# Kernel optimization log

Hardware: AMD Instinct MI355X
Metric: run time of the kernel (lower is better)

The kernel has to match this reference:

```python
import jax, jax.numpy as jnp
import numpy as np
import math

N_EMB = 256
N_HEAD = 8
B_SEGS = 128
T_SEG = 256  # equal-length segments; N = B_SEGS * T_SEG


def setup_inputs() -> dict:
    key = jax.random.key(0)
    ks = jax.random.split(key, 10)
    N = B_SEGS * T_SEG
    x = jax.random.normal(ks[0], (N, N_EMB), dtype=jnp.float32)
    batch = jnp.repeat(jnp.arange(B_SEGS, dtype=jnp.int64), T_SEG)
    s = 1.0 / math.sqrt(N_EMB)
    def lin(k):
        kw, kb = jax.random.split(k)
        W = jax.random.uniform(kw, (N_EMB, N_EMB), jnp.float32, -s, s)
        b = jax.random.uniform(kb, (N_EMB,), jnp.float32, -s, s)
        return W, b
    Wq, bq = lin(ks[1])
    Wk, bk = lin(ks[2])
    Wv, bv = lin(ks[3])
    Wp, bp = lin(ks[4])
    return {"x": x, "batch": batch, "Wq": Wq, "bq": bq, "Wk": Wk, "bk": bk,
            "Wv": Wv, "bv": bv, "Wp": Wp, "bp": bp}


def reference(x, batch, Wq, bq, Wk, bk, Wv, bv, Wp, bp):
    # Dropout layers are identity in eval / p=0.
    N, C = x.shape
    H = N_HEAD
    hd = C // H
    B = int(batch[-1]) + 1        # equal-length segments
    T = N // B
    xr = x.reshape(B, T, C)
    # per-segment QKV projections: [B,H,T,hd]
    def heads(W, b):
        return (xr @ W.T + b).reshape(B, T, H, hd).transpose(0, 2, 1, 3)
    q = heads(Wq, bq)
    k = heads(Wk, bk)
    v = heads(Wv, bv)
    scores = jnp.einsum('bhtd,bhsd->bhts', q, k) * (1.0 / math.sqrt(hd))
    attn = jax.nn.softmax(scores, axis=-1)          # [B,H,T,T]
    y = jnp.einsum('bhts,bhsd->bhtd', attn, v)      # [B,H,T,hd]
    y = y.transpose(0, 2, 1, 3).reshape(B, T, C)
    y = y @ Wp.T + bp
    attn_mean = attn.mean(axis=1)                   # head-mean per segment [B,T,T]
    return y.reshape(N, C), attn_mean
```

## Files before the change

### kernel.cpp

```cpp
#include <hip/hip_runtime.h>
#include <hip/hip_bf16.h>
#include <stdint.h>

typedef unsigned short u16;
typedef __bf16 bf16_t;
typedef bf16_t bf16x8 __attribute__((ext_vector_type(8)));
typedef float f32x4 __attribute__((ext_vector_type(4)));

#define NTOK 32768
#define CEMB 256
#define NHEAD 8
#define HD 32
#define BSEG 128
#define TSEG 256

static __device__ __forceinline__ bf16x8 ld16(const u16* p) {
  uint4 v = *reinterpret_cast<const uint4*>(p);
  return __builtin_bit_cast(bf16x8, v);
}
static __device__ __forceinline__ u16 f2b(float f) {
  return __builtin_bit_cast(u16, (bf16_t)f);
}

typedef __attribute__((address_space(1))) const void GASV;
typedef __attribute__((address_space(3))) void LASV;
static __device__ __forceinline__ void stage16(const u16* g, u16* l) {
  __builtin_amdgcn_global_load_lds((GASV*)g, (LASV*)l, 16, 0, 0);
}

__global__ void k_convert(const float* __restrict__ x,
                          const float* __restrict__ wq, const float* __restrict__ wk,
                          const float* __restrict__ wv, const float* __restrict__ wp,
                          u16* __restrict__ xb, u16* __restrict__ wb) {
  const int XSLOTS = (NTOK * CEMB) / 8;
  const int WSLOTS = (4 * CEMB * CEMB) / 8;
  int slot = blockIdx.x * blockDim.x + threadIdx.x;
  if (slot >= XSLOTS + WSLOTS) return;
  const float* src;
  u16* dst;
  if (slot < XSLOTS) {
    src = x + slot * 8;
    dst = xb + slot * 8;
  } else {
    int e = (slot - XSLOTS) * 8;
    int wsel = e >> 16, off = e & 65535;
    const float* s0 = (wsel == 0) ? wq : ((wsel == 1) ? wk : ((wsel == 2) ? wv : wp));
    src = s0 + off;
    dst = wb + e;
  }
  float4 a = reinterpret_cast<const float4*>(src)[0];
  float4 b = reinterpret_cast<const float4*>(src)[1];
  u16 o[8] = {f2b(a.x), f2b(a.y), f2b(a.z), f2b(a.w),
              f2b(b.x), f2b(b.y), f2b(b.z), f2b(b.w)};
  *reinterpret_cast<uint4*>(dst) = *reinterpret_cast<const uint4*>(o);
}

#define GEMM_MAIN_LOOP(Asrc, Bsrc)                                              \
  f32x4 acc[4][4];                                                              \
  _Pragma("unroll") for (int mf = 0; mf < 4; ++mf)                              \
      _Pragma("unroll") for (int nf = 0; nf < 4; ++nf) {                        \
    f32x4 z = {0.f, 0.f, 0.f, 0.f};                                             \
    acc[mf][nf] = z;                                                            \
  }                                                                             \
  u16* As = lds;                                                                \
  u16* Bs = lds + 16384;                                                        \
  auto STAGE = [&](int buf, int kt) {                                           \
    _Pragma("unroll") for (int i = 0; i < 4; ++i) {                             \
      int cidx = i * 256 + tid;                                                 \
      int row = cidx >> 3;                                                      \
      int scb = ((cidx & 7) << 4) ^ ((row & 7) << 4);        \
      u16* dst_lds = As + buf * 8192 + (i * 256 + w * 64) * 8;                  \
      stage16(Asrc + (size_t)(m0 + row) * CEMB + kt * 64 + (scb >> 1), dst_lds);\
      u16* dst_ldsb = Bs + buf * 8192 + (i * 256 + w * 64) * 8;                 \
      stage16(Bsrc + (size_t)(n0 + row) * CEMB + kt * 64 + (scb >> 1), dst_ldsb);\
    }                                                                           \
  };                                                                            \
  STAGE(0, 0);                                                                  \
  __syncthreads();                                                              \
  for (int kt = 0; kt < 4; ++kt) {                                              \
    int buf = kt & 1;                                                           \
    if (kt < 3) STAGE(buf ^ 1, kt + 1);                                         \
    bf16x8 av[4][2], bw[4][2];                                                  \
    _Pragma("unroll") for (int mf = 0; mf < 4; ++mf)                            \
        _Pragma("unroll") for (int kk = 0; kk < 2; ++kk) {                      \
      int row = wr * 64 + mf * 16 + lr;                                         \
      int byte = row * 128 + ((kk * 64 + lg * 16) ^ ((row & 7) << 4));          \
      av[mf][kk] = *reinterpret_cast<const bf16x8*>(                            \
          (const char*)(As + buf * 8192) + byte);                               \
    }                                                                           \
    _Pragma("unroll") for (int nf = 0; nf < 4; ++nf)                            \
        _Pragma("unroll") for (int kk = 0; kk < 2; ++kk) {                      \
      int row = wc * 64 + nf * 16 + lr;                                         \
      int byte = row * 128 + ((kk * 64 + lg * 16) ^ ((row & 7) << 4));          \
      bw[nf][kk] = *reinterpret_cast<const bf16x8*>(                            \
          (const char*)(Bs + buf * 8192) + byte);                               \
    }                                                                           \
    _Pragma("unroll") for (int kk = 0; kk < 2; ++kk)                            \
        _Pragma("unroll") for (int nf = 0; nf < 4; ++nf)                        \
            _Pragma("unroll") for (int mf = 0; mf < 4; ++mf)                    \
      acc[mf][nf] = __builtin_amdgcn_mfma_f32_16x16x32_bf16(                    \
          av[mf][kk], bw[nf][kk], acc[mf][nf], 0, 0, 0);                        \
    __syncthreads();                                                            \
  }

__global__ __launch_bounds__(256, 2)
void k_qkv(const u16* __restrict__ xb, const u16* __restrict__ wb,
           const float* __restrict__ bq, const float* __restrict__ bk,
           const float* __restrict__ bv,
           u16* __restrict__ q_ws, u16* __restrict__ k_ws, u16* __restrict__ v_ws) {
  const int d = blockIdx.x;
  const int xcd = d & 7, i = d >> 3;
  const int m_idx = xcd * 32 + i / 6;
  const int rr = i % 6;
  const int mode = rr >> 1;
  const int n0 = (rr & 1) * 128;
  const int m0 = m_idx * 128;
  const int tid = threadIdx.x;
  const int w = tid >> 6, l = tid & 63;
  const int lr = l & 15, lg = l >> 4;
  const int wr = w >> 1, wc = w & 1;

  __shared__ u16 lds[32768];

  const u16* W = wb + mode * (CEMB * CEMB);
  const float* bias = (mode == 0) ? bq : ((mode == 1) ? bk : bv);

  GEMM_MAIN_LOOP(xb, W)

  float bb[4];
#pragma unroll
  for (int nf = 0; nf < 4; ++nf) bb[nf] = bias[n0 + wc * 64 + nf * 16 + lr];

  if (mode < 2) {
    u16* Et = lds;
#pragma unroll
    for (int mf = 0; mf < 4; ++mf)
#pragma unroll
      for (int nf = 0; nf < 4; ++nf)
#pragma unroll
        for (int r = 0; r < 4; ++r) {
          int row = wr * 64 + mf * 16 + lg * 4 + r;
          int col = wc * 64 + nf * 16 + lr;
          int byte = (row * 256 + col * 2) ^ ((row & 7) << 4);
          *(u16*)((char*)Et + byte) = f2b(acc[mf][nf][r] + bb[nf]);
        }
    __syncthreads();
    u16* out = (mode == 0) ? q_ws : k_ws;
    int row_l = tid >> 1, half = tid & 1;
    u16* dstp = out + (size_t)(m0 + row_l) * CEMB + n0 + half * 64;
#pragma unroll
    for (int j = 0; j < 8; ++j) {
      int byte = row_l * 256 + (((half * 64 + j * 8) * 2) ^ ((row_l & 7) << 4));
      *reinterpret_cast<uint4*>(dstp + j * 8) =
          *reinterpret_cast<const uint4*>((const char*)Et + byte);
    }
  } else {
    u16* Vt = lds;
#pragma unroll
    for (int mf = 0; mf < 4; ++mf)
#pragma unroll
      for (int nf = 0; nf < 4; ++nf)
#pragma unroll
        for (int r = 0; r < 4; ++r) {
          int row = wr * 64 + mf * 16 + lg * 4 + r;
          int col = wc * 64 + nf * 16 + lr;
          int byte = (col * 256 + row * 2) ^ ((col & 7) << 4);
          *(u16*)((char*)Vt + byte) = f2b(acc[mf][nf][r] + bb[nf]);
        }
    __syncthreads();
    int col_l = tid >> 1, half = tid & 1;
    int c = n0 + col_l, hh = c >> 5, dd = c & 31;
    int bs = m0 >> 8, t0 = m0 & 255;
    u16* dst = v_ws + ((size_t)(bs * NHEAD + hh) * HD + dd) * TSEG + t0 + half * 64;
#pragma unroll
    for (int j = 0; j < 8; ++j) {
      int byte = col_l * 256 + ((half * 128 + j * 16) ^ ((col_l & 7) << 4));
      *reinterpret_cast<uint4*>(dst + j * 8) =
          *reinterpret_cast<const uint4*>((const char*)Vt + byte);
    }
  }
}

__global__ __launch_bounds__(512, 2)
void k_attn(const u16* __restrict__ q_ws, const u16* __restrict__ k_ws,
            const u16* __restrict__ v_ws,
            u16* __restrict__ y_ws, float* __restrict__ mean_out) {
  const int dblk = blockIdx.x;
  const int xcd = dblk & 7, ii = dblk >> 3;
  const int b = xcd * 16 + (ii >> 1);
  const int th = ii & 1;
  const int tid = threadIdx.x;
  const int w = tid >> 6, l = tid & 63;
  const int lr = l & 15, lg = l >> 4;
  const int tbase = th * 128 + w * 16;

  __shared__ u16 ldsKV[32768];

  float macc[16][4];
#pragma unroll
  for (int st = 0; st < 16; ++st)
#pragma unroll
    for (int r = 0; r < 4; ++r) macc[st][r] = 0.f;

  const float sc = 0.17677669529663687f * 1.4426950408889634f;

  const u16* qseg = q_ws + (size_t)b * TSEG * CEMB;
  const u16* kseg = k_ws + (size_t)b * TSEG * CEMB;
  const u16* vseg = v_ws + (size_t)(b * NHEAD) * HD * TSEG;

  auto STAGE_KV = [&](int hn, int bn) {
    u16* Kb = ldsKV + bn * 8192;
    u16* Vb = ldsKV + 16384 + bn * 8192;
#pragma unroll
    for (int r = 0; r < 2; ++r) {
      int idx = r * 512 + tid;
      int c = idx >> 6, l2 = idx & 63;
      int lr2 = l2 & 15, lg2 = l2 >> 4;
      int srow = 32 * (c >> 1) + 4 * (c & 1) + 8 * (lr2 >> 2) + (lr2 & 3);
      stage16(kseg + srow * CEMB + hn * HD + lg2 * 8, Kb + idx * 8);
      int vrow = (c >> 3) * 16 + lr2;
      int vcol = (c & 7) * 32 + lg2 * 8;
      stage16(vseg + (size_t)(hn * HD + vrow) * TSEG + vcol, Vb + idx * 8);
    }
  };

  STAGE_KV(0, 0);
  bf16x8 qf = ld16(qseg + (tbase + lr) * CEMB + lg * 8);

  for (int h = 0; h < NHEAD; ++h) {
    const int bn = h & 1;
    __syncthreads();
    if (h < 7) STAGE_KV(h + 1, bn ^ 1);
    const u16* Kb = ldsKV + bn * 8192;
    const u16* Vb = ldsKV + 16384 + bn * 8192;

    float s[16][4];
#pragma unroll
    for (int st = 0; st < 16; ++st) {
      bf16x8 kf = *reinterpret_cast<const bf16x8*>(Kb + (st * 64 + l) * 8);
      f32x4 z = {0.f, 0.f, 0.f, 0.f};
      f32x4 dd = __builtin_amdgcn_mfma_f32_16x16x32_bf16(kf, qf, z, 0, 0, 0);
#pragma unroll
      for (int r = 0; r < 4; ++r) s[st][r] = dd[r] * sc;
    }

    qf = ld16(qseg + (tbase + lr) * CEMB + ((h + 1) & 7) * HD + lg * 8);

    float mx = s[0][0];
#pragma unroll
    for (int st = 0; st < 16; ++st)
#pragma unroll
      for (int r = 0; r < 4; ++r) mx = fmaxf(mx, s[st][r]);
    mx = fmaxf(mx, __shfl_xor(mx, 16, 64));
    mx = fmaxf(mx, __shfl_xor(mx, 32, 64));

    float sm = 0.f;
#pragma unroll
    for (int st = 0; st < 16; ++st)
#pragma unroll
      for (int r = 0; r < 4; ++r) {
        float p = exp2f(s[st][r] - mx);
        s[st][r] = p;
        sm += p;
      }
    sm += __shfl_xor(sm, 16, 64);
    sm += __shfl_xor(sm, 32, 64);
    float inv = __builtin_amdgcn_rcpf(sm);

    bf16x8 pb[8];
#pragma unroll
    for (int kk = 0; kk < 8; ++kk)
#pragma unroll
      for (int e = 0; e < 4; ++e) {
        float p0 = s[2 * kk][e] * inv;
        float p1 = s[2 * kk + 1][e] * inv;
        macc[2 * kk][e] += p0;
        macc[2 * kk + 1][e] += p1;
        pb[kk][e] = (bf16_t)p0;
        pb[kk][4 + e] = (bf16_t)p1;
      }

#pragma unroll
    for (int dt = 0; dt < 2; ++dt) {
      f32x4 y = {0.f, 0.f, 0.f, 0.f};
#pragma unroll
      for (int kk = 0; kk < 8; ++kk) {
        bf16x8 vf = *reinterpret_cast<const bf16x8*>(Vb + ((dt * 8 + kk) * 64 + l) * 8);
        y = __builtin_amdgcn_mfma_f32_16x16x32_bf16(vf, pb[kk], y, 0, 0, 0);
      }
      u16 o[4] = {f2b(y[0]), f2b(y[1]), f2b(y[2]), f2b(y[3])};
      *reinterpret_cast<uint2*>(
          y_ws + (size_t)(b * TSEG + tbase + lr) * CEMB + h * HD + dt * 16 + lg * 4) =
          *reinterpret_cast<const uint2*>(o);
    }
  }

  __syncthreads();

  float* smem = reinterpret_cast<float*>(ldsKV);
  float* smw = smem + w * (16 * 65) + lr * 65;
  const int trow = l >> 2;
  const int cql = (l & 3) * 4;
  const float* srcp = smem + w * (16 * 65) + trow * 65 + cql;
  float* gdst = mean_out + (size_t)(b * TSEG + tbase + trow) * TSEG + cql;

  for (int c = 0; c < 4; ++c) {
#pragma unroll
    for (int j = 0; j < 2; ++j)
#pragma unroll
      for (int jj = 0; jj < 2; ++jj) {
        int st = 4 * c + 2 * j + jj;
        int sl = 32 * j + 4 * jj + 8 * lg;
#pragma unroll
        for (int r = 0; r < 4; ++r) smw[sl + r] = macc[st][r] * 0.125f;
      }
#pragma unroll
    for (int j = 0; j < 4; ++j)
      *reinterpret_cast<f32x4*>(gdst + c * 64 + j * 16) =
          *reinterpret_cast<const f32x4*>(srcp + j * 16);
  }
}

__global__ __launch_bounds__(256, 2)
void k_proj(const u16* __restrict__ yb, const u16* __restrict__ wb,
            const float* __restrict__ bp, float* __restrict__ out) {
  const int d = blockIdx.x;
  const int xcd = d & 7, i = d >> 3;
  const int m0 = (xcd * 32 + (i >> 1)) * 128;
  const int n0 = (i & 1) * 128;
  const int tid = threadIdx.x;
  const int w = tid >> 6, l = tid & 63;
  const int lr = l & 15, lg = l >> 4;
  const int wr = w >> 1, wc = w & 1;
  const u16* W = wb + 3 * (CEMB * CEMB);

  __shared__ u16 lds[32768];

  GEMM_MAIN_LOOP(yb, W)

  float bb[4];
#pragma unroll
  for (int nf = 0; nf < 4; ++nf) bb[nf] = bp[n0 + wc * 64 + nf * 16 + lr];
#pragma unroll
  for (int mf = 0; mf < 4; ++mf)
#pragma unroll
    for (int nf = 0; nf < 4; ++nf)
#pragma unroll
      for (int r = 0; r < 4; ++r) {
        int m = m0 + wr * 64 + mf * 16 + lg * 4 + r;
        int c = n0 + wc * 64 + nf * 16 + lr;
        out[(size_t)m * CEMB + c] = acc[mf][nf][r] + bb[nf];
      }
}

extern "C" void kernel_launch(void* const* d_in, const int* in_sizes, int n_in,
                              void* d_out, int out_size, void* d_ws, size_t ws_size,
                              hipStream_t stream) {
  (void)in_sizes; (void)n_in; (void)out_size; (void)ws_size;
  const float* x  = (const float*)d_in[0];
  const float* Wq = (const float*)d_in[2];
  const float* bq = (const float*)d_in[3];
  const float* Wk = (const float*)d_in[4];
  const float* bk = (const float*)d_in[5];
  const float* Wv = (const float*)d_in[6];
  const float* bv = (const float*)d_in[7];
  const float* Wp = (const float*)d_in[8];
  const float* bp = (const float*)d_in[9];
  float* out = (float*)d_out;

  char* ws = (char*)d_ws;
  u16* xb   = (u16*)(ws);
  u16* wb   = (u16*)(ws + 16777216);
  u16* q_ws = (u16*)(ws + 17301504);
  u16* k_ws = (u16*)(ws + 34078720);
  u16* v_ws = (u16*)(ws + 50855936);
  u16* y_ws = xb;
  float* mean_out = out + (size_t)NTOK * CEMB;

  k_convert<<<4224, 256, 0, stream>>>(x, Wq, Wk, Wv, Wp, xb, wb);
  k_qkv<<<1536, 256, 0, stream>>>(xb, wb, bq, bk, bv, q_ws, k_ws, v_ws);
  k_attn<<<256, 512, 0, stream>>>(q_ws, k_ws, v_ws, y_ws, mean_out);
  k_proj<<<512, 256, 0, stream>>>(y_ws, wb, bp, out);
}
```

Baseline: 93.13 us.

## Process two attention heads per iteration and fold softmax scale into Q

The attention kernel now stages K/V for two heads at a time into a larger double-buffered dynamic LDS region (128 KiB) and interleaves their QK MFMAs and exp work, to give the scheduler more independent instructions. The softmax scale is folded into the Q projection epilogue. The row-max subtraction is dropped. Normalization is deferred: the PV output is scaled after the MFMA and the head-mean is accumulated with an fma. Dropping the max makes exp overflow possible for large scores, and the bigger LDS footprint limits the kernel to one resident block per CU.

Result: slower. 99.25 us (+6.6%).

```diff
diff --git a/kernel.cpp b/kernel.cpp
--- a/kernel.cpp
+++ b/kernel.cpp
@@ -13,6 +13,8 @@
 #define HD 32
 #define BSEG 128
 #define TSEG 256
+
+#define SCQ (0.17677669529663687f * 1.4426950408889634f)
 
 static __device__ __forceinline__ bf16x8 ld16(const u16* p) {
   uint4 v = *reinterpret_cast<const uint4*>(p);
@@ -131,6 +133,8 @@
 #pragma unroll
   for (int nf = 0; nf < 4; ++nf) bb[nf] = bias[n0 + wc * 64 + nf * 16 + lr];
 
+  const float osc = (mode == 0) ? SCQ : 1.0f;
+
   if (mode < 2) {
     u16* Et = lds;
 #pragma unroll
@@ -142,7 +146,7 @@
           int row = wr * 64 + mf * 16 + lg * 4 + r;
           int col = wc * 64 + nf * 16 + lr;
           int byte = (row * 256 + col * 2) ^ ((row & 7) << 4);
-          *(u16*)((char*)Et + byte) = f2b(acc[mf][nf][r] + bb[nf]);
+          *(u16*)((char*)Et + byte) = f2b((acc[mf][nf][r] + bb[nf]) * osc);
         }
     __syncthreads();
     u16* out = (mode == 0) ? q_ws : k_ws;
@@ -194,104 +198,143 @@
   const int lr = l & 15, lg = l >> 4;
   const int tbase = th * 128 + w * 16;
 
-  __shared__ u16 ldsKV[32768];
+  extern __shared__ u16 ldsKV[];
 
   float macc[16][4];
 #pragma unroll
   for (int st = 0; st < 16; ++st)
 #pragma unroll
     for (int r = 0; r < 4; ++r) macc[st][r] = 0.f;
-
-  const float sc = 0.17677669529663687f * 1.4426950408889634f;
 
   const u16* qseg = q_ws + (size_t)b * TSEG * CEMB;
   const u16* kseg = k_ws + (size_t)b * TSEG * CEMB;
   const u16* vseg = v_ws + (size_t)(b * NHEAD) * HD * TSEG;
 
-  auto STAGE_KV = [&](int hn, int bn) {
-    u16* Kb = ldsKV + bn * 8192;
-    u16* Vb = ldsKV + 16384 + bn * 8192;
-#pragma unroll
-    for (int r = 0; r < 2; ++r) {
+  auto STAGE_PAIR = [&](int pi, int pbuf) {
+#pragma unroll
+    for (int r = 0; r < 4; ++r) {
       int idx = r * 512 + tid;
-      int c = idx >> 6, l2 = idx & 63;
+      int hs = idx >> 10;
+      int c = (idx >> 6) & 15;
+      int l2 = idx & 63;
       int lr2 = l2 & 15, lg2 = l2 >> 4;
+      int hn = pi * 2 + hs;
       int srow = 32 * (c >> 1) + 4 * (c & 1) + 8 * (lr2 >> 2) + (lr2 & 3);
-      stage16(kseg + srow * CEMB + hn * HD + lg2 * 8, Kb + idx * 8);
+      stage16(kseg + srow * CEMB + hn * HD + lg2 * 8,
+              ldsKV + ((pbuf * 2 + hs) * 1024 + c * 64 + l2) * 8);
       int vrow = (c >> 3) * 16 + lr2;
       int vcol = (c & 7) * 32 + lg2 * 8;
-      stage16(vseg + (size_t)(hn * HD + vrow) * TSEG + vcol, Vb + idx * 8);
+      stage16(vseg + (size_t)(hn * HD + vrow) * TSEG + vcol,
+              ldsKV + 32768 + ((pbuf * 2 + hs) * 1024 + c * 64 + l2) * 8);
     }
   };
 
-  STAGE_KV(0, 0);
-  bf16x8 qf = ld16(qseg + (tbase + lr) * CEMB + lg * 8);
-
-  for (int h = 0; h < NHEAD; ++h) {
-    const int bn = h & 1;
+  STAGE_PAIR(0, 0);
+  bf16x8 qa = ld16(qseg + (tbase + lr) * CEMB + 0 * HD + lg * 8);
+  bf16x8 qb = ld16(qseg + (tbase + lr) * CEMB + 1 * HD + lg * 8);
+
+  for (int i = 0; i < 4; ++i) {
+    const int pbuf = i & 1;
     __syncthreads();
-    if (h < 7) STAGE_KV(h + 1, bn ^ 1);
-    const u16* Kb = ldsKV + bn * 8192;
-    const u16* Vb = ldsKV + 16384 + bn * 8192;
-
-    float s[16][4];
+    if (i < 3) STAGE_PAIR(i + 1, pbuf ^ 1);
+    const u16* KbA = ldsKV + (pbuf * 2 + 0) * 8192;
+    const u16* KbB = ldsKV + (pbuf * 2 + 1) * 8192;
+    const u16* VbA = ldsKV + 32768 + (pbuf * 2 + 0) * 8192;
+    const u16* VbB = ldsKV + 32768 + (pbuf * 2 + 1) * 8192;
+
+    float sA[16][4], sB[16][4];
 #pragma unroll
     for (int st = 0; st < 16; ++st) {
-      bf16x8 kf = *reinterpret_cast<const bf16x8*>(Kb + (st * 64 + l) * 8);
+      bf16x8 kfA = *reinterpret_cast<const bf16x8*>(KbA + (st * 64 + l) * 8);
+      bf16x8 kfB = *reinterpret_cast<const bf16x8*>(KbB + (st * 64 + l) * 8);
       f32x4 z = {0.f, 0.f, 0.f, 0.f};
-      f32x4 dd = __builtin_amdgcn_mfma_f32_16x16x32_bf16(kf, qf, z, 0, 0, 0);
-#pragma unroll
-      for (int r = 0; r < 4; ++r) s[st][r] = dd[r] * sc;
-    }
-
-    qf = ld16(qseg + (tbase + lr) * CEMB + ((h + 1) & 7) * HD + lg * 8);
-
-    float mx = s[0][0];
-#pragma unroll
-    for (int st = 0; st < 16; ++st)
-#pragma unroll
-      for (int r = 0; r < 4; ++r) mx = fmaxf(mx, s[st][r]);
-    mx = fmaxf(mx, __shfl_xor(mx, 16, 64));
-    mx = fmaxf(mx, __shfl_xor(mx, 32, 64));
-
-    float sm = 0.f;
-#pragma unroll
-    for (int st = 0; st < 16; ++st)
-#pragma unroll
-      for (int r = 0; r < 4; ++r) {
-        float p = exp2f(s[st][r] - mx);
-        s[st][r] = p;
-        sm += p;
+      f32x4 dA = __builtin_amdgcn_mfma_f32_16x16x32_bf16(kfA, qa, z, 0, 0, 0);
+      f32x4 dB = __builtin_amdgcn_mfma_f32_16x16x32_bf16(kfB, qb, z, 0, 0, 0);
+#pragma unroll
+      for (int r = 0; r < 4; ++r) { sA[st][r] = dA[r]; sB[st][r] = dB[r]; }
+    }
+
+    {
+      const int hn0 = ((i + 1) & 3) * 2;
+      qa = ld16(qseg + (tbase + lr) * CEMB + hn0 * HD + lg * 8);
+      qb = ld16(qseg + (tbase + lr) * CEMB + (hn0 + 1) * HD + lg * 8);
+    }
+
+    float a0 = 0.f, a1 = 0.f, a2 = 0.f, a3 = 0.f;
+    float b0 = 0.f, b1 = 0.f, b2 = 0.f, b3 = 0.f;
+#pragma unroll
+    for (int st = 0; st < 16; ++st) {
+      float pa0 = exp2f(sA[st][0]), pa1 = exp2f(sA[st][1]);
+      float pa2 = exp2f(sA[st][2]), pa3 = exp2f(sA[st][3]);
+      float pb0 = exp2f(sB[st][0]), pb1 = exp2f(sB[st][1]);
+      float pb2 = exp2f(sB[st][2]), pb3 = exp2f(sB[st][3]);
+      sA[st][0] = pa0; sA[st][1] = pa1; sA[st][2] = pa2; sA[st][3] = pa3;
+      sB[st][0] = pb0; sB[st][1] = pb1; sB[st][2] = pb2; sB[st][3] = pb3;
+      a0 += pa0; a1 += pa1; a2 += pa2; a3 += pa3;
+      b0 += pb0; b1 += pb1; b2 += pb2; b3 += pb3;
+    }
+    float smA = (a0 + a1) + (a2 + a3);
+    float smB = (b0 + b1) + (b2 + b3);
+    smA += __shfl_xor(smA, 16, 64);
+    smB += __shfl_xor(smB, 16, 64);
+    smA += __shfl_xor(smA, 32, 64);
+    smB += __shfl_xor(smB, 32, 64);
+    const float invA = __builtin_amdgcn_rcpf(smA);
+    const float invB = __builtin_amdgcn_rcpf(smB);
+
+    {
+      bf16x8 pb[8];
+#pragma unroll
+      for (int kk = 0; kk < 8; ++kk)
+#pragma unroll
+        for (int e = 0; e < 4; ++e) {
+          float p0 = sA[2 * kk][e];
+          float p1 = sA[2 * kk + 1][e];
+          macc[2 * kk][e] = fmaf(p0, invA, macc[2 * kk][e]);
+          macc[2 * kk + 1][e] = fmaf(p1, invA, macc[2 * kk + 1][e]);
+          pb[kk][e] = (bf16_t)p0;
+          pb[kk][4 + e] = (bf16_t)p1;
+        }
+#pragma unroll
+      for (int dt = 0; dt < 2; ++dt) {
+        f32x4 y = {0.f, 0.f, 0.f, 0.f};
+#pragma unroll
+        for (int kk = 0; kk < 8; ++kk) {
+          bf16x8 vf = *reinterpret_cast<const bf16x8*>(VbA + ((dt * 8 + kk) * 64 + l) * 8);
+          y = __builtin_amdgcn_mfma_f32_16x16x32_bf16(vf, pb[kk], y, 0, 0, 0);
+        }
+        u16 o[4] = {f2b(y[0] * invA), f2b(y[1] * invA), f2b(y[2] * invA), f2b(y[3] * invA)};
+        *reinterpret_cast<uint2*>(
+            y_ws + (size_t)(b * TSEG + tbase + lr) * CEMB + (2 * i) * HD + dt * 16 + lg * 4) =
+            *reinterpret_cast<const uint2*>(o);
       }
-    sm += __shfl_xor(sm, 16, 64);
-    sm += __shfl_xor(sm, 32, 64);
-    float inv = __builtin_amdgcn_rcpf(sm);
-
-    bf16x8 pb[8];
-#pragma unroll
-    for (int kk = 0; kk < 8; ++kk)
-#pragma unroll
-      for (int e = 0; e < 4; ++e) {
-        float p0 = s[2 * kk][e] * inv;
-        float p1 = s[2 * kk + 1][e] * inv;
-        macc[2 * kk][e] += p0;
-        macc[2 * kk + 1][e] += p1;
-        pb[kk][e] = (bf16_t)p0;
-        pb[kk][4 + e] = (bf16_t)p1;
+    }
+    {
+      bf16x8 pb[8];
+#pragma unroll
+      for (int kk = 0; kk < 8; ++kk)
+#pragma unroll
+        for (int e = 0; e < 4; ++e) {
+          float p0 = sB[2 * kk][e];
+          float p1 = sB[2 * kk + 1][e];
+          macc[2 * kk][e] = fmaf(p0, invB, macc[2 * kk][e]);
+          macc[2 * kk + 1][e] = fmaf(p1, invB, macc[2 * kk + 1][e]);
+          pb[kk][e] = (bf16_t)p0;
+          pb[kk][4 + e] = (bf16_t)p1;
+        }
+#pragma unroll
+      for (int dt = 0; dt < 2; ++dt) {
+        f32x4 y = {0.f, 0.f, 0.f, 0.f};
+#pragma unroll
+        for (int kk = 0; kk < 8; ++kk) {
+          bf16x8 vf = *reinterpret_cast<const bf16x8*>(VbB + ((dt * 8 + kk) * 64 + l) * 8);
+          y = __builtin_amdgcn_mfma_f32_16x16x32_bf16(vf, pb[kk], y, 0, 0, 0);
+        }
+        u16 o[4] = {f2b(y[0] * invB), f2b(y[1] * invB), f2b(y[2] * invB), f2b(y[3] * invB)};
+        *reinterpret_cast<uint2*>(
+            y_ws + (size_t)(b * TSEG + tbase + lr) * CEMB + (2 * i + 1) * HD + dt * 16 + lg * 4) =
+            *reinterpret_cast<const uint2*>(o);
       }
-
-#pragma unroll
-    for (int dt = 0; dt < 2; ++dt) {
-      f32x4 y = {0.f, 0.f, 0.f, 0.f};
-#pragma unroll
-      for (int kk = 0; kk < 8; ++kk) {
-        bf16x8 vf = *reinterpret_cast<const bf16x8*>(Vb + ((dt * 8 + kk) * 64 + l) * 8);
-        y = __builtin_amdgcn_mfma_f32_16x16x32_bf16(vf, pb[kk], y, 0, 0, 0);
-      }
-      u16 o[4] = {f2b(y[0]), f2b(y[1]), f2b(y[2]), f2b(y[3])};
-      *reinterpret_cast<uint2*>(
-          y_ws + (size_t)(b * TSEG + tbase + lr) * CEMB + h * HD + dt * 16 + lg * 4) =
-          *reinterpret_cast<const uint2*>(o);
     }
   }
 
@@ -379,6 +422,6 @@
 
   k_convert<<<4224, 256, 0, stream>>>(x, Wq, Wk, Wv, Wp, xb, wb);
   k_qkv<<<1536, 256, 0, stream>>>(xb, wb, bq, bk, bv, q_ws, k_ws, v_ws);
-  k_attn<<<256, 512, 0, stream>>>(q_ws, k_ws, v_ws, y_ws, mean_out);
+  k_attn<<<256, 512, 131072, stream>>>(q_ws, k_ws, v_ws, y_ws, mean_out);
   k_proj<<<512, 256, 0, stream>>>(y_ws, wb, bp, out);
 }
```
